# Kernel optimization log

Hardware: AMD Instinct MI355X
Metric: run time of the kernel (lower is better)

The kernel has to match this reference:

```python
import jax, jax.numpy as jnp
import numpy as np

T, B, H, K = 512, 64, 512, 16  # seq_len, batch, hidden_size, num_tags


def setup_inputs() -> dict:
    key = jax.random.key(0)
    ks = jax.random.split(key, 8)
    hidden = jax.random.normal(ks[0], (T, B, H), dtype=jnp.float32)
    W1 = jax.random.normal(ks[1], (H, H), dtype=jnp.float32) / np.float32(np.sqrt(H))
    b1 = jnp.zeros((H,), jnp.float32)
    W2 = jax.random.normal(ks[2], (H, K), dtype=jnp.float32) / np.float32(np.sqrt(H))
    b2 = jnp.zeros((K,), jnp.float32)
    transition = jax.random.normal(ks[3], (K, K), dtype=jnp.float32)
    lens = jax.random.randint(ks[4], (B,), T // 2, T + 1)  # valid lengths in [T/2, T]
    tags = jax.random.randint(ks[5], (T, B), 0, K)
    return dict(hidden=hidden, W1=W1, b1=b1, W2=W2, b2=b2,
                transition=transition, lens=lens, tags=tags)


def reference(hidden, W1, b1, W2, b2, transition, lens, tags):
    # Emission MLP (dropout is identity in eval): Linear -> ReLU -> Linear
    h = jax.nn.relu(hidden @ W1 + b1)          # [T, B, H]
    em = h @ W2 + b2                           # [T, B, K]

    # ---- forward (partition) score: linear-chain logsumexp DP ----
    def step(alpha, e_t):
        # alpha: [B, K] over prev tags; transition[curr, prev]
        a = jax.nn.logsumexp(alpha[:, None, :] + transition[None, :, :], axis=-1) + e_t
        return a, a

    alpha0 = em[0]
    _, alphas = jax.lax.scan(step, alpha0, em[1:])
    alphas = jnp.concatenate([alpha0[None], alphas], axis=0)            # [T, B, K]
    last = jnp.take_along_axis(alphas, (lens - 1)[None, :, None], axis=0)[0]  # [B, K]
    fwd_score = jax.nn.logsumexp(last, axis=-1)                          # [B]

    # ---- gold path score ----
    em_path = jnp.take_along_axis(em, tags[:, :, None], axis=-1)[..., 0]  # [T, B]
    trans_path = transition[tags[1:], tags[:-1]]                          # [T-1, B]
    steps = em_path.at[1:].add(trans_path)
    cum = jnp.cumsum(steps, axis=0)                                       # [T, B]
    gold = jnp.take_along_axis(cum, (lens - 1)[None, :], axis=0)[0]       # [B]

    return (fwd_score - gold).sum()
```

## Files before the change

kernel.cpp:

```cpp
#include <hip/hip_runtime.h>
#include <hip/hip_bf16.h>

#define TT 512
#define BB 64
#define HH 512
#define KK 16

typedef __attribute__((ext_vector_type(8))) short bf16x8;
typedef __attribute__((ext_vector_type(4))) short bf16x4;
typedef __attribute__((ext_vector_type(4))) float f32x4;

#define MFMA_K16(A, B, C) __builtin_amdgcn_mfma_f32_16x16x16bf16_1k(A, B, C, 0, 0, 0)

__device__ __forceinline__ unsigned short f2bf(float f) {
    union { __hip_bfloat16 h; unsigned short u; } cvt;
    cvt.h = __float2bfloat16(f);
    return cvt.u;
}

__device__ __forceinline__ short rne_bf(float x) {
    unsigned u = __float_as_uint(x);
    u += 0x7fffu + ((u >> 16) & 1u);
    return (short)(u >> 16);
}

__device__ __forceinline__ float bf2f(short s) {
    return __uint_as_float(((unsigned)(unsigned short)s) << 16);
}

__global__ void prep_kernel(const float* __restrict__ W1, const float* __restrict__ W2,
                            unsigned short* __restrict__ W1t, unsigned short* __restrict__ W2t,
                            float* __restrict__ out) {
    const int bi = blockIdx.x, tx = threadIdx.x;
    if (bi < 64) {
        __shared__ float Ls[64][65];
        const int ti = bi & 7, tj = bi >> 3;
        const int r0 = ti * 64, c0 = tj * 64;
        const int r = tx >> 4, c4 = (tx & 15) * 4;
#pragma unroll
        for (int i = 0; i < 4; ++i) {
            float4 v = *(const float4*)(W1 + (size_t)(r0 + r + 16 * i) * HH + c0 + c4);
            Ls[c4 + 0][r + 16 * i] = v.x;
            Ls[c4 + 1][r + 16 * i] = v.y;
            Ls[c4 + 2][r + 16 * i] = v.z;
            Ls[c4 + 3][r + 16 * i] = v.w;
        }
        __syncthreads();
        const int rn = tx >> 4, k4 = (tx & 15) * 4;
#pragma unroll
        for (int i = 0; i < 4; ++i) {
            const int n = rn + 16 * i;
            ushort4 o;
            o.x = f2bf(Ls[n][k4 + 0]);
            o.y = f2bf(Ls[n][k4 + 1]);
            o.z = f2bf(Ls[n][k4 + 2]);
            o.w = f2bf(Ls[n][k4 + 3]);
            *(ushort4*)(W1t + (size_t)(c0 + n) * HH + r0 + k4) = o;
        }
    } else {
        if (tx == 0) out[0] = 0.0f;
        for (int idx = tx; idx < 16 * HH; idx += 256) {
            const int n = idx >> 9, k = idx & 511;
            W2t[idx] = f2bf(W2[k * KK + n]);
        }
    }
}

__global__ __launch_bounds__(256, 2)
void em_kernel(const float* __restrict__ hidden, const unsigned short* __restrict__ W1t,
               const float* __restrict__ b1, const unsigned short* __restrict__ W2t,
               const float* __restrict__ b2, float* __restrict__ em) {
    __shared__ unsigned short W2ts[16 * 520];
    __shared__ __align__(16) unsigned char stage[37888];
    unsigned short* As = (unsigned short*)stage;
    unsigned short* Bs = (unsigned short*)(stage + 5120);
    unsigned short* Hb = (unsigned short*)stage;

    const int tx = threadIdx.x;
    const int w = tx >> 6, lane = tx & 63;
    const int q = lane >> 4, nl = lane & 15;
    const int wm = w >> 1, wn = w & 1;
    const int row0 = blockIdx.x * 64;

    for (int i = tx; i < 16 * 64; i += 256) {
        const int n = i >> 6, kc = i & 63;
        *(bf16x8*)(W2ts + n * 520 + kc * 8) = *(const bf16x8*)(W2t + n * HH + kc * 8);
    }

    f32x4 acc[2][16];
#pragma unroll
    for (int mt = 0; mt < 2; ++mt)
#pragma unroll
        for (int nt = 0; nt < 16; ++nt) acc[mt][nt] = (f32x4){0.f, 0.f, 0.f, 0.f};

    for (int kt = 0; kt < 16; ++kt) {
        const int k0 = kt * 32;
        __syncthreads();
        {
            const int r = tx >> 2, c8 = (tx & 3) * 8;
            const float* src = hidden + (size_t)(row0 + r) * HH + k0 + c8;
            float4 v0 = *(const float4*)(src);
            float4 v1 = *(const float4*)(src + 4);
            bf16x8 o;
            o[0] = (short)f2bf(v0.x); o[1] = (short)f2bf(v0.y);
            o[2] = (short)f2bf(v0.z); o[3] = (short)f2bf(v0.w);
            o[4] = (short)f2bf(v1.x); o[5] = (short)f2bf(v1.y);
            o[6] = (short)f2bf(v1.z); o[7] = (short)f2bf(v1.w);
            *(bf16x8*)(As + r * 40 + c8) = o;
        }
#pragma unroll
        for (int it = 0; it < 8; ++it) {
            const int c = it * 256 + tx;
            const int n = c >> 2, slot = c & 3;
            const int kc = slot ^ ((n >> 1) & 3);
            __builtin_amdgcn_global_load_lds(
                (const __attribute__((address_space(1))) void*)(W1t + (size_t)n * HH + k0 + kc * 8),
                (__attribute__((address_space(3))) void*)(Bs + c * 8),
                16, 0, 0);
        }
        __syncthreads();
        bf16x8 af[2];
#pragma unroll
        for (int mt = 0; mt < 2; ++mt)
            af[mt] = *(const bf16x8*)(As + (32 * wm + 16 * mt + nl) * 40 + q * 8);
#pragma unroll
        for (int nt = 0; nt < 16; ++nt) {
            const int n = 256 * wn + 16 * nt + nl;
            const int slot = q ^ ((n >> 1) & 3);
            bf16x8 bf = *(const bf16x8*)(Bs + n * 32 + slot * 8);
            acc[0][nt] = __builtin_amdgcn_mfma_f32_16x16x32_bf16(af[0], bf, acc[0][nt], 0, 0, 0);
            acc[1][nt] = __builtin_amdgcn_mfma_f32_16x16x32_bf16(af[1], bf, acc[1][nt], 0, 0, 0);
        }
    }

    f32x4 acc2 = (f32x4){0.f, 0.f, 0.f, 0.f};
    for (int c = 0; c < 2; ++c) {
        __syncthreads();
        if (wn == c) {
#pragma unroll
            for (int nt = 0; nt < 16; ++nt) {
                const float bv = b1[c * 256 + 16 * nt + nl];
#pragma unroll
                for (int mt = 0; mt < 2; ++mt) {
#pragma unroll
                    for (int r = 0; r < 4; ++r) {
                        float v = acc[mt][nt][r] + bv;
                        v = v > 0.f ? v : 0.f;
                        const int row = 32 * wm + 16 * mt + q * 4 + r;
                        Hb[row * 264 + nt * 16 + nl] = f2bf(v);
                    }
                }
            }
        }
        __syncthreads();
#pragma unroll
        for (int ks = 0; ks < 8; ++ks) {
            bf16x8 a2 = *(const bf16x8*)(Hb + (16 * w + nl) * 264 + ks * 32 + q * 8);
            bf16x8 b2f = *(const bf16x8*)(W2ts + nl * 520 + c * 256 + ks * 32 + q * 8);
            acc2 = __builtin_amdgcn_mfma_f32_16x16x32_bf16(a2, b2f, acc2, 0, 0, 0);
        }
    }
#pragma unroll
    for (int r = 0; r < 4; ++r) {
        const int row = row0 + 16 * w + q * 4 + r;
        em[(size_t)row * KK + nl] = acc2[r] + b2[nl];
    }
}

__global__ void gold_kernel(const float* __restrict__ em, const float* __restrict__ trans,
                            const int* __restrict__ lens, const int* __restrict__ tags,
                            float* __restrict__ out) {
    __shared__ float trs[256];
    __shared__ float red[4];
    const int tid = threadIdx.x;
    trs[tid] = __logf(bf2f(rne_bf(__expf(trans[tid]))));
    __syncthreads();
    const int idx = blockIdx.x * 256 + tid;
    const int t = idx >> 6, b = idx & 63;
    const int L = lens[b];
    float v = 0.0f;
    if (t < L) {
        const int tg = tags[t * BB + b];
        v = em[((size_t)t * BB + b) * KK + tg];
        if (t > 0) v += trs[tg * 16 + tags[(t - 1) * BB + b]];
    }
#pragma unroll
    for (int dd = 1; dd < 64; dd <<= 1) v += __shfl_xor(v, dd, 64);
    if ((tid & 63) == 0) red[tid >> 6] = v;
    __syncthreads();
    if (tid == 0) atomicAdd(out, -(red[0] + red[1] + red[2] + red[3]));
}

__global__ void chunk_kernel(const float* __restrict__ em, const float* __restrict__ trans,
                             const int* __restrict__ lens,
                             float* __restrict__ Pfull, float* __restrict__ Cfull,
                             float* __restrict__ Ppart, float* __restrict__ Cpart) {
    const int tx = threadIdx.x;
    const int id = blockIdx.x * 4 + (tx >> 6);
    const int lane = tx & 63, q = lane >> 4, col = lane & 15;
    const int b = id >> 3, c = id & 7;

    float mf[4];
    {
        float4 tv = *(const float4*)(trans + col * 16 + 4 * q);
        mf[0] = bf2f(rne_bf(__expf(tv.x)));
        mf[1] = bf2f(rne_bf(__expf(tv.y)));
        mf[2] = bf2f(rne_bf(__expf(tv.z)));
        mf[3] = bf2f(rne_bf(__expf(tv.w)));
    }
    const int Lm1 = lens[b] - 1;
    const int tb0 = 64 * c;

    float ebuf[8];
#pragma unroll
    for (int i = 0; i < 8; ++i)
        ebuf[i] = em[(size_t)((tb0 + i) * BB + b) * KK + col];

    bf16x4 gb;
#pragma unroll
    for (int i = 0; i < 4; ++i)
        gb[i] = (4 * q + i == col) ? rne_bf(1.0f) : (short)0;

    const f32x4 zc = (f32x4){0.f, 0.f, 0.f, 0.f};
    f32x4 d = (f32x4){0.f, 0.f, 0.f, 0.f};
    float K = 1.0f, rk = 1.0f, lk = 0.0f, Cacc = 0.0f;

    for (int sb = 0; sb < 64; sb += 8) {
        const bool refill = (sb < 56);
#pragma unroll
        for (int s8 = 0; s8 < 8; ++s8) {
            const int t = tb0 + sb + s8;
            const float eraw = ebuf[s8];
            if (refill)
                ebuf[s8] = em[(size_t)((t + 8) * BB + b) * KK + col];
            float ev = __expf(eraw);
            if ((s8 & 3) == 0 && (sb + s8) >= 4) {
                ev *= rk;
                Cacc += lk;
            }
            bf16x4 af;
            af[0] = rne_bf(ev * mf[0]); af[1] = rne_bf(ev * mf[1]);
            af[2] = rne_bf(ev * mf[2]); af[3] = rne_bf(ev * mf[3]);
            if (s8 == 0) {
                if (sb == 0 && c == 0) {
#pragma unroll
                    for (int i = 0; i < 4; ++i)
                        af[i] = (4 * q + i == col) ? rne_bf(ev) : (short)0;
                }
            }
            d = MFMA_K16(af, gb, zc);
            if ((s8 & 3) == 1) {
                K = __shfl(d[0], 0, 64);
                const float Km = fmaxf(K, 1e-30f);
                rk = 1.0f / Km;
                lk = __logf(Km);
            }
            if (t == Lm1) {
#pragma unroll
                for (int r = 0; r < 4; ++r)
                    Ppart[b * 256 + (4 * q + r) * 16 + col] = d[r];
                if (lane == 0) Cpart[b] = Cacc;
            }
            gb[0] = rne_bf(d[0]); gb[1] = rne_bf(d[1]);
            gb[2] = rne_bf(d[2]); gb[3] = rne_bf(d[3]);
        }
    }
#pragma unroll
    for (int r = 0; r < 4; ++r)
        Pfull[(size_t)(b * 8 + c) * 256 + (4 * q + r) * 16 + col] = d[r];
    if (lane == 0) Cfull[b * 8 + c] = Cacc;
}

__global__ void combine_kernel(const int* __restrict__ lens,
                               const float* __restrict__ Pfull, const float* __restrict__ Cfull,
                               const float* __restrict__ Ppart, const float* __restrict__ Cpart,
                               float* __restrict__ out) {
    const int lane = threadIdx.x;
    const int grp = lane >> 4, j = lane & 15;
    const int b = blockIdx.x * 4 + grp;
    const int base = grp << 4;
    const int cstar = (lens[b] - 1) >> 6;

    float g = 1.0f, acc = 0.0f;
    for (int c = 0; c < 8; ++c) {
        const bool act = (c <= cstar);
        const float* P = (c < cstar) ? (Pfull + (size_t)(b * 8 + c) * 256)
                                     : (Ppart + b * 256);
        float gn = 0.0f;
#pragma unroll
        for (int k = 0; k < 16; ++k) {
            const float gk = __shfl(g, base + k, 64);
            gn += P[j * 16 + k] * gk;
        }
        if (act) {
            float m = gn;
#pragma unroll
            for (int dd = 1; dd < 16; dd <<= 1) m = fmaxf(m, __shfl_xor(m, dd, 64));
            g = gn / m;
            acc += __logf(m) + ((c < cstar) ? Cfull[b * 8 + c] : Cpart[b]);
        }
    }
    float ssum = g;
#pragma unroll
    for (int dd = 1; dd < 16; dd <<= 1) ssum += __shfl_xor(ssum, dd, 64);
    const float fwd = acc + __logf(ssum);
    if (j == 0) atomicAdd(out, fwd);
}

extern "C" void kernel_launch(void* const* d_in, const int* in_sizes, int n_in,
                              void* d_out, int out_size, void* d_ws, size_t ws_size,
                              hipStream_t stream) {
    const float* hidden = (const float*)d_in[0];
    const float* W1     = (const float*)d_in[1];
    const float* b1     = (const float*)d_in[2];
    const float* W2     = (const float*)d_in[3];
    const float* b2     = (const float*)d_in[4];
    const float* trans  = (const float*)d_in[5];
    const int*   lens   = (const int*)d_in[6];
    const int*   tags   = (const int*)d_in[7];
    float* out = (float*)d_out;

    char* ws = (char*)d_ws;
    float* em = (float*)ws;
    unsigned short* W1t = (unsigned short*)(ws + 2097152);
    unsigned short* W2t = (unsigned short*)(ws + 2621440);
    float* Pfull = (float*)(ws + 2637824);
    float* Cfull = (float*)(ws + 3162112);
    float* Ppart = (float*)(ws + 3164160);
    float* Cpart = (float*)(ws + 3229696);

    prep_kernel<<<65, 256, 0, stream>>>(W1, W2, W1t, W2t, out);
    em_kernel<<<512, 256, 0, stream>>>(hidden, W1t, b1, W2t, b2, em);
    gold_kernel<<<128, 256, 0, stream>>>(em, trans, lens, tags, out);
    chunk_kernel<<<128, 256, 0, stream>>>(em, trans, lens, Pfull, Cfull, Ppart, Cpart);
    combine_kernel<<<16, 64, 0, stream>>>(lens, Pfull, Cfull, Ppart, Cpart, out);
}
```

Before: 165.1 us.

## Pre-swizzle W1 into MFMA fragment layout, drop LDS staging, rechunk CRF scan, fuse gold

W1 is now stored in MFMA fragment order, so em_kernel loads A and B operands straight from global memory into registers with no LDS staging or barriers in the K loop. The block shrinks to 2 waves, each computing 64x256 with 64 accumulators. The forward scan is split into 16 chunks of 32 steps instead of 8 of 64, doubling parallelism. The gold-path score is folded into the combine kernel, removing one launch. Pfull now aliases the W1f workspace region, which is safe only because em_kernel finishes before chunk_kernel writes. The trade-off is high register pressure and fewer waves per CU in the GEMM.

```diff
diff --git a/kernel.cpp b/kernel.cpp
--- a/kernel.cpp
+++ b/kernel.cpp
@@ -11,6 +11,7 @@
 typedef __attribute__((ext_vector_type(4))) float f32x4;
 
 #define MFMA_K16(A, B, C) __builtin_amdgcn_mfma_f32_16x16x16bf16_1k(A, B, C, 0, 0, 0)
+#define MFMA_K32(A, B, C) __builtin_amdgcn_mfma_f32_16x16x32_bf16(A, B, C, 0, 0, 0)
 
 __device__ __forceinline__ unsigned short f2bf(float f) {
     union { __hip_bfloat16 h; unsigned short u; } cvt;
@@ -29,7 +30,7 @@
 }
 
 __global__ void prep_kernel(const float* __restrict__ W1, const float* __restrict__ W2,
-                            unsigned short* __restrict__ W1t, unsigned short* __restrict__ W2t,
+                            unsigned short* __restrict__ W1f, unsigned short* __restrict__ W2t,
                             float* __restrict__ out) {
     const int bi = blockIdx.x, tx = threadIdx.x;
     if (bi < 64) {
@@ -46,16 +47,20 @@
             Ls[c4 + 3][r + 16 * i] = v.w;
         }
         __syncthreads();
-        const int rn = tx >> 4, k4 = (tx & 15) * 4;
-#pragma unroll
-        for (int i = 0; i < 4; ++i) {
-            const int n = rn + 16 * i;
-            ushort4 o;
-            o.x = f2bf(Ls[n][k4 + 0]);
-            o.y = f2bf(Ls[n][k4 + 1]);
-            o.z = f2bf(Ls[n][k4 + 2]);
-            o.w = f2bf(Ls[n][k4 + 3]);
-            *(ushort4*)(W1t + (size_t)(c0 + n) * HH + r0 + k4) = o;
+#pragma unroll
+        for (int p = 0; p < 2; ++p) {
+            const int flat = p * 256 + tx;
+            const int tl = flat >> 6;
+            const int lane = flat & 63;
+            const int q = lane >> 4, nl = lane & 15;
+            const int ktl = tl >> 2, gl = tl & 3;
+            const int kt = ti * 2 + ktl;
+            const int gnt = tj * 4 + gl;
+            const int nloc = 16 * gl + nl, kloc = 32 * ktl + 8 * q;
+            bf16x8 o;
+#pragma unroll
+            for (int i = 0; i < 8; ++i) o[i] = (short)f2bf(Ls[nloc][kloc + i]);
+            *(bf16x8*)(W1f + ((size_t)(kt * 32 + gnt) * 64 + lane) * 8) = o;
         }
     } else {
         if (tx == 0) out[0] = 0.0f;
@@ -66,74 +71,51 @@
     }
 }
 
-__global__ __launch_bounds__(256, 2)
-void em_kernel(const float* __restrict__ hidden, const unsigned short* __restrict__ W1t,
+__global__ __launch_bounds__(128, 1)
+void em_kernel(const float* __restrict__ hidden, const unsigned short* __restrict__ W1f,
                const float* __restrict__ b1, const unsigned short* __restrict__ W2t,
                const float* __restrict__ b2, float* __restrict__ em) {
-    __shared__ unsigned short W2ts[16 * 520];
-    __shared__ __align__(16) unsigned char stage[37888];
-    unsigned short* As = (unsigned short*)stage;
-    unsigned short* Bs = (unsigned short*)(stage + 5120);
-    unsigned short* Hb = (unsigned short*)stage;
+    __shared__ unsigned short Hb[64 * 264];
 
     const int tx = threadIdx.x;
-    const int w = tx >> 6, lane = tx & 63;
+    const int wn = tx >> 6, lane = tx & 63;
     const int q = lane >> 4, nl = lane & 15;
-    const int wm = w >> 1, wn = w & 1;
     const int row0 = blockIdx.x * 64;
 
-    for (int i = tx; i < 16 * 64; i += 256) {
-        const int n = i >> 6, kc = i & 63;
-        *(bf16x8*)(W2ts + n * 520 + kc * 8) = *(const bf16x8*)(W2t + n * HH + kc * 8);
-    }
-
-    f32x4 acc[2][16];
-#pragma unroll
-    for (int mt = 0; mt < 2; ++mt)
+    f32x4 acc[4][16];
+#pragma unroll
+    for (int mt = 0; mt < 4; ++mt)
 #pragma unroll
         for (int nt = 0; nt < 16; ++nt) acc[mt][nt] = (f32x4){0.f, 0.f, 0.f, 0.f};
 
     for (int kt = 0; kt < 16; ++kt) {
-        const int k0 = kt * 32;
-        __syncthreads();
-        {
-            const int r = tx >> 2, c8 = (tx & 3) * 8;
-            const float* src = hidden + (size_t)(row0 + r) * HH + k0 + c8;
-            float4 v0 = *(const float4*)(src);
-            float4 v1 = *(const float4*)(src + 4);
+        bf16x8 a[4];
+#pragma unroll
+        for (int mt = 0; mt < 4; ++mt) {
+            const float* ap = hidden + (size_t)(row0 + 16 * mt + nl) * HH + kt * 32 + q * 8;
+            float4 v0 = *(const float4*)(ap);
+            float4 v1 = *(const float4*)(ap + 4);
             bf16x8 o;
             o[0] = (short)f2bf(v0.x); o[1] = (short)f2bf(v0.y);
             o[2] = (short)f2bf(v0.z); o[3] = (short)f2bf(v0.w);
             o[4] = (short)f2bf(v1.x); o[5] = (short)f2bf(v1.y);
             o[6] = (short)f2bf(v1.z); o[7] = (short)f2bf(v1.w);
-            *(bf16x8*)(As + r * 40 + c8) = o;
-        }
-#pragma unroll
-        for (int it = 0; it < 8; ++it) {
-            const int c = it * 256 + tx;
-            const int n = c >> 2, slot = c & 3;
-            const int kc = slot ^ ((n >> 1) & 3);
-            __builtin_amdgcn_global_load_lds(
-                (const __attribute__((address_space(1))) void*)(W1t + (size_t)n * HH + k0 + kc * 8),
-                (__attribute__((address_space(3))) void*)(Bs + c * 8),
-                16, 0, 0);
-        }
-        __syncthreads();
-        bf16x8 af[2];
-#pragma unroll
-        for (int mt = 0; mt < 2; ++mt)
-            af[mt] = *(const bf16x8*)(As + (32 * wm + 16 * mt + nl) * 40 + q * 8);
-#pragma unroll
-        for (int nt = 0; nt < 16; ++nt) {
-            const int n = 256 * wn + 16 * nt + nl;
-            const int slot = q ^ ((n >> 1) & 3);
-            bf16x8 bf = *(const bf16x8*)(Bs + n * 32 + slot * 8);
-            acc[0][nt] = __builtin_amdgcn_mfma_f32_16x16x32_bf16(af[0], bf, acc[0][nt], 0, 0, 0);
-            acc[1][nt] = __builtin_amdgcn_mfma_f32_16x16x32_bf16(af[1], bf, acc[1][nt], 0, 0, 0);
-        }
-    }
-
-    f32x4 acc2 = (f32x4){0.f, 0.f, 0.f, 0.f};
+            a[mt] = o;
+        }
+        const bf16x8* bp = (const bf16x8*)W1f + (size_t)(kt * 32 + wn * 16) * 64 + lane;
+        bf16x8 b[16];
+#pragma unroll
+        for (int nt = 0; nt < 16; ++nt) b[nt] = bp[nt * 64];
+#pragma unroll
+        for (int nt = 0; nt < 16; ++nt)
+#pragma unroll
+            for (int mt = 0; mt < 4; ++mt)
+                acc[mt][nt] = MFMA_K32(a[mt], b[nt], acc[mt][nt]);
+    }
+
+    f32x4 acc2[2];
+    acc2[0] = (f32x4){0.f, 0.f, 0.f, 0.f};
+    acc2[1] = (f32x4){0.f, 0.f, 0.f, 0.f};
     for (int c = 0; c < 2; ++c) {
         __syncthreads();
         if (wn == c) {
@@ -141,13 +123,12 @@
             for (int nt = 0; nt < 16; ++nt) {
                 const float bv = b1[c * 256 + 16 * nt + nl];
 #pragma unroll
-                for (int mt = 0; mt < 2; ++mt) {
+                for (int mt = 0; mt < 4; ++mt) {
 #pragma unroll
                     for (int r = 0; r < 4; ++r) {
                         float v = acc[mt][nt][r] + bv;
                         v = v > 0.f ? v : 0.f;
-                        const int row = 32 * wm + 16 * mt + q * 4 + r;
-                        Hb[row * 264 + nt * 16 + nl] = f2bf(v);
+                        Hb[(16 * mt + 4 * q + r) * 264 + nt * 16 + nl] = f2bf(v);
                     }
                 }
             }
@@ -155,40 +136,21 @@
         __syncthreads();
 #pragma unroll
         for (int ks = 0; ks < 8; ++ks) {
-            bf16x8 a2 = *(const bf16x8*)(Hb + (16 * w + nl) * 264 + ks * 32 + q * 8);
-            bf16x8 b2f = *(const bf16x8*)(W2ts + nl * 520 + c * 256 + ks * 32 + q * 8);
-            acc2 = __builtin_amdgcn_mfma_f32_16x16x32_bf16(a2, b2f, acc2, 0, 0, 0);
-        }
-    }
-#pragma unroll
-    for (int r = 0; r < 4; ++r) {
-        const int row = row0 + 16 * w + q * 4 + r;
-        em[(size_t)row * KK + nl] = acc2[r] + b2[nl];
-    }
-}
-
-__global__ void gold_kernel(const float* __restrict__ em, const float* __restrict__ trans,
-                            const int* __restrict__ lens, const int* __restrict__ tags,
-                            float* __restrict__ out) {
-    __shared__ float trs[256];
-    __shared__ float red[4];
-    const int tid = threadIdx.x;
-    trs[tid] = __logf(bf2f(rne_bf(__expf(trans[tid]))));
-    __syncthreads();
-    const int idx = blockIdx.x * 256 + tid;
-    const int t = idx >> 6, b = idx & 63;
-    const int L = lens[b];
-    float v = 0.0f;
-    if (t < L) {
-        const int tg = tags[t * BB + b];
-        v = em[((size_t)t * BB + b) * KK + tg];
-        if (t > 0) v += trs[tg * 16 + tags[(t - 1) * BB + b]];
-    }
-#pragma unroll
-    for (int dd = 1; dd < 64; dd <<= 1) v += __shfl_xor(v, dd, 64);
-    if ((tid & 63) == 0) red[tid >> 6] = v;
-    __syncthreads();
-    if (tid == 0) atomicAdd(out, -(red[0] + red[1] + red[2] + red[3]));
+            bf16x8 b2f = *(const bf16x8*)(W2t + nl * HH + c * 256 + ks * 32 + q * 8);
+#pragma unroll
+            for (int mt2 = 0; mt2 < 2; ++mt2) {
+                bf16x8 a2 = *(const bf16x8*)(Hb + (32 * wn + 16 * mt2 + nl) * 264 + ks * 32 + q * 8);
+                acc2[mt2] = MFMA_K32(a2, b2f, acc2[mt2]);
+            }
+        }
+    }
+#pragma unroll
+    for (int mt2 = 0; mt2 < 2; ++mt2)
+#pragma unroll
+        for (int r = 0; r < 4; ++r) {
+            const int row = row0 + 32 * wn + 16 * mt2 + 4 * q + r;
+            em[(size_t)row * KK + nl] = acc2[mt2][r] + b2[nl];
+        }
 }
 
 __global__ void chunk_kernel(const float* __restrict__ em, const float* __restrict__ trans,
@@ -198,7 +160,7 @@
     const int tx = threadIdx.x;
     const int id = blockIdx.x * 4 + (tx >> 6);
     const int lane = tx & 63, q = lane >> 4, col = lane & 15;
-    const int b = id >> 3, c = id & 7;
+    const int c = id >> 6, b = id & 63;
 
     float mf[4];
     {
@@ -209,7 +171,7 @@
         mf[3] = bf2f(rne_bf(__expf(tv.w)));
     }
     const int Lm1 = lens[b] - 1;
-    const int tb0 = 64 * c;
+    const int tb0 = 32 * c;
 
     float ebuf[8];
 #pragma unroll
@@ -225,8 +187,8 @@
     f32x4 d = (f32x4){0.f, 0.f, 0.f, 0.f};
     float K = 1.0f, rk = 1.0f, lk = 0.0f, Cacc = 0.0f;
 
-    for (int sb = 0; sb < 64; sb += 8) {
-        const bool refill = (sb < 56);
+    for (int sb = 0; sb < 32; sb += 8) {
+        const bool refill = (sb < 24);
 #pragma unroll
         for (int s8 = 0; s8 < 8; ++s8) {
             const int t = tb0 + sb + s8;
@@ -241,12 +203,10 @@
             bf16x4 af;
             af[0] = rne_bf(ev * mf[0]); af[1] = rne_bf(ev * mf[1]);
             af[2] = rne_bf(ev * mf[2]); af[3] = rne_bf(ev * mf[3]);
-            if (s8 == 0) {
-                if (sb == 0 && c == 0) {
-#pragma unroll
-                    for (int i = 0; i < 4; ++i)
-                        af[i] = (4 * q + i == col) ? rne_bf(ev) : (short)0;
-                }
+            if (sb == 0 && s8 == 0 && c == 0) {
+#pragma unroll
+                for (int i = 0; i < 4; ++i)
+                    af[i] = (4 * q + i == col) ? rne_bf(ev) : (short)0;
             }
             d = MFMA_K16(af, gb, zc);
             if ((s8 & 3) == 1) {
@@ -267,44 +227,67 @@
     }
 #pragma unroll
     for (int r = 0; r < 4; ++r)
-        Pfull[(size_t)(b * 8 + c) * 256 + (4 * q + r) * 16 + col] = d[r];
-    if (lane == 0) Cfull[b * 8 + c] = Cacc;
-}
-
-__global__ void combine_kernel(const int* __restrict__ lens,
+        Pfull[(size_t)(b * 16 + c) * 256 + (4 * q + r) * 16 + col] = d[r];
+    if (lane == 0) Cfull[b * 16 + c] = Cacc;
+}
+
+__global__ void combine_kernel(const float* __restrict__ em, const float* __restrict__ trans,
+                               const int* __restrict__ lens, const int* __restrict__ tags,
                                const float* __restrict__ Pfull, const float* __restrict__ Cfull,
                                const float* __restrict__ Ppart, const float* __restrict__ Cpart,
                                float* __restrict__ out) {
-    const int lane = threadIdx.x;
-    const int grp = lane >> 4, j = lane & 15;
-    const int b = blockIdx.x * 4 + grp;
-    const int base = grp << 4;
-    const int cstar = (lens[b] - 1) >> 6;
-
-    float g = 1.0f, acc = 0.0f;
-    for (int c = 0; c < 8; ++c) {
-        const bool act = (c <= cstar);
-        const float* P = (c < cstar) ? (Pfull + (size_t)(b * 8 + c) * 256)
-                                     : (Ppart + b * 256);
-        float gn = 0.0f;
-#pragma unroll
-        for (int k = 0; k < 16; ++k) {
-            const float gk = __shfl(g, base + k, 64);
-            gn += P[j * 16 + k] * gk;
-        }
-        if (act) {
-            float m = gn;
-#pragma unroll
-            for (int dd = 1; dd < 16; dd <<= 1) m = fmaxf(m, __shfl_xor(m, dd, 64));
-            g = gn / m;
-            acc += __logf(m) + ((c < cstar) ? Cfull[b * 8 + c] : Cpart[b]);
-        }
-    }
-    float ssum = g;
-#pragma unroll
-    for (int dd = 1; dd < 16; dd <<= 1) ssum += __shfl_xor(ssum, dd, 64);
-    const float fwd = acc + __logf(ssum);
-    if (j == 0) atomicAdd(out, fwd);
+    __shared__ float trs[256];
+    __shared__ float red[4];
+    const int b = blockIdx.x, tid = threadIdx.x;
+    trs[tid] = __logf(bf2f(rne_bf(__expf(trans[tid]))));
+    __syncthreads();
+    const int L = lens[b];
+    float v = 0.0f;
+#pragma unroll
+    for (int p = 0; p < 2; ++p) {
+        const int t = p * 256 + tid;
+        if (t < L) {
+            const int tg = tags[t * BB + b];
+            float u = em[((size_t)t * BB + b) * KK + tg];
+            if (t > 0) u += trs[tg * 16 + tags[(t - 1) * BB + b]];
+            v += u;
+        }
+    }
+#pragma unroll
+    for (int dd = 1; dd < 64; dd <<= 1) v += __shfl_xor(v, dd, 64);
+    if ((tid & 63) == 0) red[tid >> 6] = v;
+    __syncthreads();
+
+    if (tid < 64) {
+        const int j = tid & 15;
+        const int base = (tid >> 4) << 4;
+        const int cstar = (lens[b] - 1) >> 5;
+        float g = 1.0f, acc = 0.0f;
+        for (int c = 0; c < 16; ++c) {
+            const bool act = (c <= cstar);
+            const float* P = (c < cstar) ? (Pfull + (size_t)(b * 16 + c) * 256)
+                                         : (Ppart + b * 256);
+            float gn = 0.0f;
+#pragma unroll
+            for (int k = 0; k < 16; ++k) {
+                const float gk = __shfl(g, base + k, 64);
+                gn += P[j * 16 + k] * gk;
+            }
+            if (act) {
+                float m = gn;
+#pragma unroll
+                for (int dd = 1; dd < 16; dd <<= 1) m = fmaxf(m, __shfl_xor(m, dd, 64));
+                g = gn / m;
+                acc += __logf(m) + ((c < cstar) ? Cfull[b * 16 + c] : Cpart[b]);
+            }
+        }
+        float ssum = g;
+#pragma unroll
+        for (int dd = 1; dd < 16; dd <<= 1) ssum += __shfl_xor(ssum, dd, 64);
+        const float fwd = acc + __logf(ssum);
+        if (tid == 0)
+            atomicAdd(out, fwd - (red[0] + red[1] + red[2] + red[3]));
+    }
 }
 
 extern "C" void kernel_launch(void* const* d_in, const int* in_sizes, int n_in,
@@ -322,16 +305,15 @@
 
     char* ws = (char*)d_ws;
     float* em = (float*)ws;
-    unsigned short* W1t = (unsigned short*)(ws + 2097152);
+    unsigned short* W1f = (unsigned short*)(ws + 2097152);
     unsigned short* W2t = (unsigned short*)(ws + 2621440);
-    float* Pfull = (float*)(ws + 2637824);
-    float* Cfull = (float*)(ws + 3162112);
-    float* Ppart = (float*)(ws + 3164160);
-    float* Cpart = (float*)(ws + 3229696);
-
-    prep_kernel<<<65, 256, 0, stream>>>(W1, W2, W1t, W2t, out);
-    em_kernel<<<512, 256, 0, stream>>>(hidden, W1t, b1, W2t, b2, em);
-    gold_kernel<<<128, 256, 0, stream>>>(em, trans, lens, tags, out);
-    chunk_kernel<<<128, 256, 0, stream>>>(em, trans, lens, Pfull, Cfull, Ppart, Cpart);
-    combine_kernel<<<16, 64, 0, stream>>>(lens, Pfull, Cfull, Ppart, Cpart, out);
-}
+    float* Pfull = (float*)(ws + 2097152);
+    float* Cfull = (float*)(ws + 3145728);
+    float* Ppart = (float*)(ws + 3149824);
+    float* Cpart = (float*)(ws + 3215360);
+
+    prep_kernel<<<65, 256, 0, stream>>>(W1, W2, W1f, W2t, out);
+    em_kernel<<<512, 128, 0, stream>>>(hidden, W1f, b1, W2t, b2, em);
+    chunk_kernel<<<256, 256, 0, stream>>>(em, trans, lens, Pfull, Cfull, Ppart, Cpart);
+    combine_kernel<<<64, 256, 0, stream>>>(em, trans, lens, tags, Pfull, Cfull, Ppart, Cpart, out);
+}
```

After: 176.4 us. 1.07x slower.
